# Performance work log

Measured on AMD Instinct MI355X. Metric: run time of the kernel, lower is better.

The kernel has to match this reference:

```python
import jax, jax.numpy as jnp
import numpy as np

N, E = 16384, 262144
IN, H, OUT = 128, 256, 256
L, HEADS = 4, 8
OC = H // HEADS  # 32, also MHA head_dim
B, NB = 64, 256  # graphs, nodes per graph (N = B*NB, equal-size graphs)


def _ln(x, g, b, eps=1e-5):
    m = x.mean(-1, keepdims=True)
    v = ((x - m) ** 2).mean(-1, keepdims=True)
    return (x - m) / jnp.sqrt(v + eps) * g + b


def setup_inputs() -> dict:
    key = jax.random.key(0)
    ks = iter(jax.random.split(key, 40))
    r = lambda *s: jax.random.normal(next(ks), s, jnp.float32) * 0.05
    return dict(
        x=jax.random.normal(next(ks), (N, IN), jnp.float32),
        edge_index=jax.random.randint(next(ks), (2, E), 0, N),
        wi=r(IN, H), bi=r(H),
        wg=r(L, H, H), asrc=r(L, HEADS, OC), adst=r(L, HEADS, OC), bg=r(L, H),
        g1=jnp.ones((L, H)), b1=jnp.zeros((L, H)),
        inw=r(L, 3 * H, H), inb=r(L, 3 * H), ow=r(L, H, H), ob=r(L, H),
        g2=jnp.ones((L, H)), b2=jnp.zeros((L, H)),
        mw1=r(L, H, 2 * H), mb1=r(L, 2 * H), mw2=r(L, 2 * H, H), mb2=r(L, H),
        g3=jnp.ones((L, H)), b3=jnp.zeros((L, H)),
        gf=jnp.ones(H), bf=jnp.zeros(H),
        wo=r(H, OUT), bo=r(OUT),
    )


def reference(x, edge_index, wi, bi, wg, asrc, adst, bg, g1, b1, inw, inb,
              ow, ob, g2, b2, mw1, mb1, mw2, mb2, g3, b3, gf, bf, wo, bo):
    src, dst = edge_index[0], edge_index[1]
    x = jax.nn.relu(x @ wi + bi)  # [N, H]
    for i in range(L):
        # ---- GATConv (local MPNN), eval mode (no dropout) ----
        xw = (x @ wg[i]).reshape(N, HEADS, OC)
        a = (xw * asrc[i]).sum(-1)[src] + (xw * adst[i]).sum(-1)[dst]  # [E, HEADS]
        a = jax.nn.leaky_relu(a, 0.2)
        amax = jax.ops.segment_max(a, dst, num_segments=N)
        ae = jnp.exp(a - amax[dst])
        asum = jax.ops.segment_sum(ae, dst, num_segments=N)
        attn = ae / asum[dst]  # edge softmax per destination node
        h = jax.ops.segment_sum(attn[:, :, None] * xw[src], dst, num_segments=N)
        h = h.reshape(N, H) + bg[i]
        h = _ln(h + x, g1[i], b1[i])  # GPSConv local branch + residual + norm1
        # ---- global MultiheadAttention over dense batch (equal-size graphs) ----
        xd = x.reshape(B, NB, H)
        qkv = xd @ inw[i].T + inb[i]
        q, k, v = jnp.split(qkv, 3, axis=-1)
        q = q.reshape(B, NB, HEADS, OC).transpose(0, 2, 1, 3)
        k = k.reshape(B, NB, HEADS, OC).transpose(0, 2, 1, 3)
        v = v.reshape(B, NB, HEADS, OC).transpose(0, 2, 1, 3)
        p = jax.nn.softmax(jnp.einsum('bhqd,bhkd->bhqk', q, k) / jnp.sqrt(jnp.float32(OC)), axis=-1)
        o = jnp.einsum('bhqk,bhkd->bhqd', p, v).transpose(0, 2, 1, 3).reshape(B, NB, H)
        o = (o @ ow[i].T + ob[i]).reshape(N, H)
        h2 = _ln(o + x, g2[i], b2[i])  # global branch + residual + norm2
        out = h + h2
        out = out + (jax.nn.relu(out @ mw1[i] + mb1[i]) @ mw2[i] + mb2[i])  # MLP residual
        x = _ln(out, g3[i], b3[i])  # norm3
    x = _ln(x, gf, bf)
    return x @ wo + bo
```

## Files before the change

kernel.cpp:

```cpp
#include <hip/hip_runtime.h>
#include <hip/hip_bf16.h>

#define NNODES 16384
#define NEDGES 262144
#define IND    128
#define HD     256
#define OUTDIM 256
#define LAYERS 4
#define NHEADS 8
#define OCD    32
#define NGRAPH 64
#define NBATCH 256
#define XQSTR  1024

typedef __hip_bfloat16 bf16;
typedef __attribute__((ext_vector_type(8))) short bf16x8;
typedef __attribute__((ext_vector_type(4))) short s16x4;
typedef __attribute__((ext_vector_type(4))) float f32x4;

__device__ __forceinline__ short bfbits(float v) {
    bf16 h = __float2bfloat16(v);
    return *(short*)&h;
}
__device__ __forceinline__ float b2f(short s) {
    return __uint_as_float(((unsigned)(unsigned short)s) << 16);
}

__device__ __forceinline__ size_t bidx(int row, int col, int KC) {
    return ((size_t)((row >> 6) * KC + (col >> 3)) << 9) + ((row & 63) << 3) + (col & 7);
}

__device__ __forceinline__ void gload_lds16(const short* g, short* l) {
    __builtin_amdgcn_global_load_lds(
        (const __attribute__((address_space(1))) void*)g,
        (__attribute__((address_space(3))) void*)l, 16, 0, 0);
}

#define PREP_TOTAL (32768 + NNODES*IND + IND*HD + LAYERS*1024*HD + LAYERS*1024 \
                    + LAYERS*HD*HD + LAYERS*HD*2*HD + LAYERS*2*HD*HD + HD*OUTDIM)
__global__ void prep_kernel(const float* __restrict__ x0, const float* __restrict__ wi,
                            const float* __restrict__ inw, const float* __restrict__ wg,
                            const float* __restrict__ inb, const float* __restrict__ ow,
                            const float* __restrict__ mw1, const float* __restrict__ mw2,
                            const float* __restrict__ wo,
                            short* __restrict__ x016, short* __restrict__ wi_t,
                            short* __restrict__ wcomb, float* __restrict__ cbias,
                            short* __restrict__ ow_c, short* __restrict__ mw1_t,
                            short* __restrict__ mw2_t, short* __restrict__ wo_t,
                            int* __restrict__ cnt, int* __restrict__ fill)
{
    int i = blockIdx.x * blockDim.x + threadIdx.x;
    if (i < 32768) {
        if (i < NNODES) cnt[i] = 0; else fill[i - NNODES] = 0;
        return;
    }
    i -= 32768;
    if (i < NNODES * IND) {
        int row = i / IND, col = i % IND;
        x016[bidx(row, col, 16)] = bfbits(x0[i]);
        return;
    }
    i -= NNODES * IND;
    if (i < IND * HD) {
        int k = i / HD, n = i % HD;
        wi_t[bidx(n, k, 16)] = bfbits(wi[i]);
        return;
    }
    i -= IND * HD;
    if (i < LAYERS * 1024 * HD) {
        int l = i >> 18, r = (i >> 8) & 1023, k = i & 255;
        float v = (r < 768) ? inw[(size_t)l * 768 * 256 + r * 256 + k]
                            : wg[(size_t)l * 256 * 256 + k * 256 + (r - 768)];
        wcomb[((size_t)l << 18) + bidx(r, k, 32)] = bfbits(v);
        return;
    }
    i -= LAYERS * 1024 * HD;
    if (i < LAYERS * 1024) {
        int l = i >> 10, c = i & 1023;
        cbias[i] = (c < 768) ? inb[l * 768 + c] : 0.f;
        return;
    }
    i -= LAYERS * 1024;
    if (i < LAYERS * HD * HD) {
        int l = i >> 16, rem = i & 65535, r = rem >> 8, k = rem & 255;
        ow_c[((size_t)l << 16) + bidx(r, k, 32)] = bfbits(ow[i]);
        return;
    }
    i -= LAYERS * HD * HD;
    if (i < LAYERS * HD * 2 * HD) {
        int l = i / (HD * 2 * HD), rem = i % (HD * 2 * HD);
        int k = rem / (2 * HD), n = rem % (2 * HD);
        mw1_t[(size_t)l * HD * 2 * HD + bidx(n, k, 32)] = bfbits(mw1[i]);
        return;
    }
    i -= LAYERS * HD * 2 * HD;
    if (i < LAYERS * 2 * HD * HD) {
        int l = i / (2 * HD * HD), rem = i % (2 * HD * HD);
        int k = rem / HD, n = rem % HD;
        mw2_t[(size_t)l * 2 * HD * HD + bidx(n, k, 64)] = bfbits(mw2[i]);
        return;
    }
    i -= LAYERS * 2 * HD * HD;
    if (i < HD * OUTDIM) {
        int k = i / OUTDIM, n = i % OUTDIM;
        wo_t[bidx(n, k, 32)] = bfbits(wo[i]);
    }
}

__global__ void hist_kernel(const int* __restrict__ dst, int* __restrict__ cnt)
{
    int e = blockIdx.x * blockDim.x + threadIdx.x;
    if (e < NEDGES) atomicAdd(&cnt[dst[e]], 1);
}

__global__ void scan_kernel(const int* __restrict__ cnt, int* __restrict__ row_ptr)
{
    __shared__ int part[256];
    int t = threadIdx.x;
    const int PER = NNODES / 256;
    int base = t * PER;
    int s = 0;
    for (int i = 0; i < PER; i++) s += cnt[base + i];
    part[t] = s;
    __syncthreads();
    for (int off = 1; off < 256; off <<= 1) {
        int v = (t >= off) ? part[t - off] : 0;
        __syncthreads();
        part[t] += v;
        __syncthreads();
    }
    int run = (t == 0) ? 0 : part[t - 1];
    for (int i = 0; i < PER; i++) { row_ptr[base + i] = run; run += cnt[base + i]; }
    if (t == 255) row_ptr[NNODES] = run;
}

__global__ void scatter_kernel(const int* __restrict__ src, const int* __restrict__ dst,
                               const int* __restrict__ row_ptr, int* __restrict__ fill,
                               int* __restrict__ srcs)
{
    int e = blockIdx.x * blockDim.x + threadIdx.x;
    if (e >= NEDGES) return;
    int d = dst[e];
    int pos = row_ptr[d] + atomicAdd(&fill[d], 1);
    srcs[pos] = src[e];
}

__global__ void gat_scores_kernel(const short* __restrict__ xw16,
                                  const float* __restrict__ asrc, const float* __restrict__ adst,
                                  float* __restrict__ ssrc, float* __restrict__ sdst)
{
    int i = blockIdx.x * blockDim.x + threadIdx.x;
    if (i >= NNODES * NHEADS) return;
    int n = i >> 3, h = i & 7;
    const bf16x8* xr = (const bf16x8*)(xw16 + (size_t)n * XQSTR + h * OCD);
    float s1 = 0.f, s2 = 0.f;
#pragma unroll
    for (int g = 0; g < 4; g++) {
        bf16x8 v8 = xr[g];
#pragma unroll
        for (int j = 0; j < 8; j++) {
            float v = b2f(v8[j]);
            int d = g * 8 + j;
            s1 += v * asrc[h * OCD + d];
            s2 += v * adst[h * OCD + d];
        }
    }
    ssrc[i] = s1;
    sdst[i] = s2;
}

__global__ __launch_bounds__(256)
void gat_agg_ln_kernel(const int* __restrict__ row_ptr, const int* __restrict__ srcs,
                       const float* __restrict__ ssrc, const float* __restrict__ sdst,
                       const short* __restrict__ xw16, const float* __restrict__ xcur,
                       const float* __restrict__ colbias, const float* __restrict__ gamma,
                       const float* __restrict__ beta, float* __restrict__ out)
{
    int wave = threadIdx.x >> 6, lane = threadIdx.x & 63;
    int n = blockIdx.x * 4 + wave;
    int c0 = lane << 2;
    int h = c0 >> 5;
    int start = row_ptr[n];
    int deg = row_ptr[n + 1] - start;
    float sd = sdst[n * NHEADS + h];

    float ax = 0.f, ay = 0.f, az = 0.f, aw = 0.f, l = 0.f;
    int j = 0;
    for (; j + 4 <= deg; j += 4) {
        int e0 = srcs[start + j + 0], e1 = srcs[start + j + 1];
        int e2 = srcs[start + j + 2], e3 = srcs[start + j + 3];
        s16x4 r0 = *(const s16x4*)&xw16[(size_t)e0 * XQSTR + c0];
        s16x4 r1 = *(const s16x4*)&xw16[(size_t)e1 * XQSTR + c0];
        s16x4 r2 = *(const s16x4*)&xw16[(size_t)e2 * XQSTR + c0];
        s16x4 r3 = *(const s16x4*)&xw16[(size_t)e3 * XQSTR + c0];
        float a0 = ssrc[e0 * NHEADS + h] + sd; a0 = a0 > 0.f ? a0 : 0.2f * a0;
        float a1 = ssrc[e1 * NHEADS + h] + sd; a1 = a1 > 0.f ? a1 : 0.2f * a1;
        float a2 = ssrc[e2 * NHEADS + h] + sd; a2 = a2 > 0.f ? a2 : 0.2f * a2;
        float a3 = ssrc[e3 * NHEADS + h] + sd; a3 = a3 > 0.f ? a3 : 0.2f * a3;
        float p0 = __expf(a0), p1 = __expf(a1), p2 = __expf(a2), p3 = __expf(a3);
        l += (p0 + p1) + (p2 + p3);
        ax += p0 * b2f(r0[0]) + p1 * b2f(r1[0]) + p2 * b2f(r2[0]) + p3 * b2f(r3[0]);
        ay += p0 * b2f(r0[1]) + p1 * b2f(r1[1]) + p2 * b2f(r2[1]) + p3 * b2f(r3[1]);
        az += p0 * b2f(r0[2]) + p1 * b2f(r1[2]) + p2 * b2f(r2[2]) + p3 * b2f(r3[2]);
        aw += p0 * b2f(r0[3]) + p1 * b2f(r1[3]) + p2 * b2f(r2[3]) + p3 * b2f(r3[3]);
    }
    for (; j < deg; j++) {
        int e0 = srcs[start + j];
        s16x4 r0 = *(const s16x4*)&xw16[(size_t)e0 * XQSTR + c0];
        float a0 = ssrc[e0 * NHEADS + h] + sd; a0 = a0 > 0.f ? a0 : 0.2f * a0;
        float p0 = __expf(a0);
        l += p0;
        ax += p0 * b2f(r0[0]); ay += p0 * b2f(r0[1]);
        az += p0 * b2f(r0[2]); aw += p0 * b2f(r0[3]);
    }
    float invl = deg ? 1.f / l : 0.f;
    size_t base = (size_t)n * HD + c0;
    float4 x4 = *(const float4*)&xcur[base];
    float4 cb = *(const float4*)&colbias[c0];
    float4 v;
    v.x = ax * invl + x4.x + cb.x;
    v.y = ay * invl + x4.y + cb.y;
    v.z = az * invl + x4.z + cb.z;
    v.w = aw * invl + x4.w + cb.w;
    float s = v.x + v.y + v.z + v.w;
    float q = v.x * v.x + v.y * v.y + v.z * v.z + v.w * v.w;
#pragma unroll
    for (int off = 1; off < 64; off <<= 1) {
        s += __shfl_xor(s, off);
        q += __shfl_xor(q, off);
    }
    float mean = s * (1.f / HD);
    float var  = fmaxf(q * (1.f / HD) - mean * mean, 0.f);
    float inv  = rsqrtf(var + 1e-5f);
    float4 g  = *(const float4*)&gamma[c0];
    float4 bt = *(const float4*)&beta[c0];
    float4 y;
    y.x = (v.x - mean) * inv * g.x + bt.x;
    y.y = (v.y - mean) * inv * g.y + bt.y;
    y.z = (v.z - mean) * inv * g.z + bt.z;
    y.w = (v.w - mean) * inv * g.w + bt.w;
    *(float4*)&out[base] = y;
}

#define GBM 128
#define GBK 32

template<int TN>
__global__ __launch_bounds__(256)
void gemm_mfma_kernel(const short* __restrict__ A16, const short* __restrict__ B16,
                      const float* __restrict__ bias, const float* __restrict__ resid,
                      float* __restrict__ Cf, short* __restrict__ C16,
                      int M, int Nc, int K, int relu, int c16rm)
{
    constexpr int NTF = TN / 32;
    __shared__ short As[GBM * GBK];
    __shared__ short Bs[TN * GBK];
    int tid = threadIdx.x;
    int wid = tid >> 6, lane = tid & 63;
    int quad = lane >> 4, l16 = lane & 15;
    int wm = wid >> 1, wn = wid & 1;
    int rowBase = blockIdx.y * GBM;
    int colBase = blockIdx.x * TN;
    int KC = K >> 3;

    f32x4 acc[4][NTF];
#pragma unroll
    for (int mt = 0; mt < 4; mt++)
#pragma unroll
        for (int nt = 0; nt < NTF; nt++) acc[mt][nt] = (f32x4)(0.f);

    const short* Ag0 = A16 + (((size_t)(blockIdx.y * 2 + 0) * KC + wid) << 9) + lane * 8;
    const short* Ag1 = A16 + (((size_t)(blockIdx.y * 2 + 1) * KC + wid) << 9) + lane * 8;
    const short* Bg0 = B16 + (((size_t)((colBase >> 6) + 0) * KC + wid) << 9) + lane * 8;
    const short* Bg1 = (TN == 128) ?
        B16 + (((size_t)((colBase >> 6) + 1) * KC + wid) << 9) + lane * 8 : nullptr;
    short* AsD0 = As + (wid * 128 + 0) * 8;
    short* AsD1 = As + (wid * 128 + 64) * 8;
    short* BsD0 = Bs + (wid * TN) * 8;
    short* BsD1 = Bs + (wid * TN + 64) * 8;

    for (int t = 0; t < (K >> 5); t++) {
        gload_lds16(Ag0 + t * 2048, AsD0);
        gload_lds16(Ag1 + t * 2048, AsD1);
        gload_lds16(Bg0 + t * 2048, BsD0);
        if (TN == 128) gload_lds16(Bg1 + t * 2048, BsD1);
        __syncthreads();
        bf16x8 aF[4], bF[NTF];
#pragma unroll
        for (int mt = 0; mt < 4; mt++)
            aF[mt] = *(bf16x8*)&As[(quad * 128 + wm * 64 + mt * 16 + l16) * 8];
#pragma unroll
        for (int nt = 0; nt < NTF; nt++)
            bF[nt] = *(bf16x8*)&Bs[(quad * TN + wn * (TN / 2) + nt * 16 + l16) * 8];
#pragma unroll
        for (int mt = 0; mt < 4; mt++)
#pragma unroll
            for (int nt = 0; nt < NTF; nt++)
                acc[mt][nt] = __builtin_amdgcn_mfma_f32_16x16x32_bf16(
                    bF[nt], aF[mt], acc[mt][nt], 0, 0, 0);
        __syncthreads();
    }

#pragma unroll
    for (int mt = 0; mt < 4; mt++) {
        int row = rowBase + wm * 64 + mt * 16 + l16;
#pragma unroll
        for (int nt = 0; nt < NTF; nt++) {
            int col0 = colBase + wn * (TN / 2) + nt * 16 + quad * 4;
            f32x4 v = acc[mt][nt];
            if (bias) {
                float4 b4 = *(const float4*)&bias[col0];
                v[0] += b4.x; v[1] += b4.y; v[2] += b4.z; v[3] += b4.w;
            }
            if (resid) {
                float4 r4 = *(const float4*)&resid[(size_t)row * Nc + col0];
                v[0] += r4.x; v[1] += r4.y; v[2] += r4.z; v[3] += r4.w;
            }
            if (relu) {
                v[0] = fmaxf(v[0], 0.f); v[1] = fmaxf(v[1], 0.f);
                v[2] = fmaxf(v[2], 0.f); v[3] = fmaxf(v[3], 0.f);
            }
            if (Cf) {
                float4 o; o.x = v[0]; o.y = v[1]; o.z = v[2]; o.w = v[3];
                *(float4*)&Cf[(size_t)row * Nc + col0] = o;
            }
            if (C16) {
                s16x4 o;
                o[0] = bfbits(v[0]); o[1] = bfbits(v[1]);
                o[2] = bfbits(v[2]); o[3] = bfbits(v[3]);
                if (c16rm) *(s16x4*)&C16[(size_t)row * Nc + col0] = o;
                else       *(s16x4*)&C16[bidx(row, col0, Nc >> 3)] = o;
            }
        }
    }
}

__global__ __launch_bounds__(256)
void gemm_ln_kernel(const short* __restrict__ A16, const short* __restrict__ B16,
                    const float* __restrict__ bias, const float* __restrict__ resid,
                    const float* __restrict__ gamma, const float* __restrict__ beta,
                    const float* __restrict__ postadd,
                    float* __restrict__ outf, short* __restrict__ out16, int K)
{
    __shared__ short As[64 * GBK];
    __shared__ short Bs[256 * GBK];
    int tid = threadIdx.x;
    int wid = tid >> 6, lane = tid & 63;
    int quad = lane >> 4, l16 = lane & 15;
    int rowBase = blockIdx.y * 64;
    int KC = K >> 3;

    f32x4 acc[16];
#pragma unroll
    for (int nt = 0; nt < 16; nt++) acc[nt] = (f32x4)(0.f);

    const short* Ag  = A16 + (((size_t)blockIdx.y * KC + wid) << 9) + lane * 8;
    const short* Bg0 = B16 + (((size_t)0 * KC + wid) << 9) + lane * 8;
    const short* Bg1 = B16 + (((size_t)1 * KC + wid) << 9) + lane * 8;
    const short* Bg2 = B16 + (((size_t)2 * KC + wid) << 9) + lane * 8;
    const short* Bg3 = B16 + (((size_t)3 * KC + wid) << 9) + lane * 8;
    short* AsD  = As + (wid * 64) * 8;
    short* BsD0 = Bs + (wid * 256 + 0) * 8;
    short* BsD1 = Bs + (wid * 256 + 64) * 8;
    short* BsD2 = Bs + (wid * 256 + 128) * 8;
    short* BsD3 = Bs + (wid * 256 + 192) * 8;

    for (int t = 0; t < (K >> 5); t++) {
        gload_lds16(Ag + t * 2048, AsD);
        gload_lds16(Bg0 + t * 2048, BsD0);
        gload_lds16(Bg1 + t * 2048, BsD1);
        gload_lds16(Bg2 + t * 2048, BsD2);
        gload_lds16(Bg3 + t * 2048, BsD3);
        __syncthreads();
        bf16x8 aF = *(bf16x8*)&As[(quad * 64 + wid * 16 + l16) * 8];
#pragma unroll
        for (int nt = 0; nt < 16; nt++) {
            bf16x8 bF = *(bf16x8*)&Bs[(quad * 256 + nt * 16 + l16) * 8];
            acc[nt] = __builtin_amdgcn_mfma_f32_16x16x32_bf16(bF, aF, acc[nt], 0, 0, 0);
        }
        __syncthreads();
    }

    int row = rowBase + wid * 16 + l16;
    float s = 0.f, q = 0.f;
#pragma unroll
    for (int nt = 0; nt < 16; nt++) {
        int col0 = nt * 16 + quad * 4;
        f32x4 v = acc[nt];
        float4 b4 = *(const float4*)&bias[col0];
        float4 r4 = *(const float4*)&resid[(size_t)row * HD + col0];
        v[0] += b4.x + r4.x; v[1] += b4.y + r4.y;
        v[2] += b4.z + r4.z; v[3] += b4.w + r4.w;
        acc[nt] = v;
        s += (v[0] + v[1]) + (v[2] + v[3]);
        q += (v[0] * v[0] + v[1] * v[1]) + (v[2] * v[2] + v[3] * v[3]);
    }
    s += __shfl_xor(s, 16); s += __shfl_xor(s, 32);
    q += __shfl_xor(q, 16); q += __shfl_xor(q, 32);
    float mean = s * (1.f / HD);
    float var  = fmaxf(q * (1.f / HD) - mean * mean, 0.f);
    float inv  = rsqrtf(var + 1e-5f);
#pragma unroll
    for (int nt = 0; nt < 16; nt++) {
        int col0 = nt * 16 + quad * 4;
        f32x4 v = acc[nt];
        float4 g4 = *(const float4*)&gamma[col0];
        float4 bt = *(const float4*)&beta[col0];
        float4 y;
        y.x = (v[0] - mean) * inv * g4.x + bt.x;
        y.y = (v[1] - mean) * inv * g4.y + bt.y;
        y.z = (v[2] - mean) * inv * g4.z + bt.z;
        y.w = (v[3] - mean) * inv * g4.w + bt.w;
        if (postadd) {
            float4 p4 = *(const float4*)&postadd[(size_t)row * HD + col0];
            y.x += p4.x; y.y += p4.y; y.z += p4.z; y.w += p4.w;
        }
        *(float4*)&outf[(size_t)row * HD + col0] = y;
        s16x4 o;
        o[0] = bfbits(y.x); o[1] = bfbits(y.y); o[2] = bfbits(y.z); o[3] = bfbits(y.w);
        *(s16x4*)&out16[bidx(row, col0, 32)] = o;
    }
}

__global__ __launch_bounds__(256)
void ln4_kernel(const float* __restrict__ in, const float* __restrict__ res,
                const float* __restrict__ gamma, const float* __restrict__ beta,
                const float* __restrict__ postadd,
                float* __restrict__ outf, short* __restrict__ out16)
{
    int wave = threadIdx.x >> 6, lane = threadIdx.x & 63;
    int row = blockIdx.x * 4 + wave;
    size_t base = (size_t)row * HD + lane * 4;
    float4 v = *(const float4*)&in[base];
    if (res) {
        float4 r = *(const float4*)&res[base];
        v.x += r.x; v.y += r.y; v.z += r.z; v.w += r.w;
    }
    float s = v.x + v.y + v.z + v.w;
    float q = v.x * v.x + v.y * v.y + v.z * v.z + v.w * v.w;
#pragma unroll
    for (int off = 1; off < 64; off <<= 1) {
        s += __shfl_xor(s, off);
        q += __shfl_xor(q, off);
    }
    float mean = s * (1.f / HD);
    float var  = fmaxf(q * (1.f / HD) - mean * mean, 0.f);
    float inv  = rsqrtf(var + 1e-5f);
    float4 g  = *(const float4*)&gamma[lane * 4];
    float4 bt = *(const float4*)&beta[lane * 4];
    float4 y;
    y.x = (v.x - mean) * inv * g.x + bt.x;
    y.y = (v.y - mean) * inv * g.y + bt.y;
    y.z = (v.z - mean) * inv * g.z + bt.z;
    y.w = (v.w - mean) * inv * g.w + bt.w;
    if (postadd) {
        float4 p = *(const float4*)&postadd[base];
        y.x += p.x; y.y += p.y; y.z += p.z; y.w += p.w;
    }
    if (outf) *(float4*)&outf[base] = y;
    if (out16) {
        s16x4 o;
        o[0] = bfbits(y.x); o[1] = bfbits(y.y); o[2] = bfbits(y.z); o[3] = bfbits(y.w);
        *(s16x4*)&out16[bidx(row, lane * 4, 32)] = o;
    }
}

#define PSTR 72
__global__ __launch_bounds__(256)
void mha_mfma_kernel(const short* __restrict__ qkv16, short* __restrict__ o16)
{
    __shared__ short smem[4 * 64 * PSTR + 32 * PSTR];
    short* VT = smem + 4 * 64 * PSTR;

    int b = blockIdx.x, h = blockIdx.y;
    int tid = threadIdx.x;
    int wid = tid >> 6, lane = tid & 63;
    int quad = lane >> 4, l16 = lane & 15;
    int base = b * NBATCH;
    int qrow0 = wid * 64;
    short* Pme = smem + wid * 64 * PSTR;

    const float scale2 = 0.17677669529663687f * 1.4426950408889634f;

    bf16x8 qA[4];
#pragma unroll
    for (int mt = 0; mt < 4; mt++)
        qA[mt] = *(const bf16x8*)&qkv16[(size_t)(base + qrow0 + mt * 16 + l16) * XQSTR + h * 32 + quad * 8];

    f32x4 accO[4][2];
#pragma unroll
    for (int mt = 0; mt < 4; mt++)
#pragma unroll
        for (int dt = 0; dt < 2; dt++) accO[mt][dt] = (f32x4)(0.f);
    float lsum[4][4];
#pragma unroll
    for (int mt = 0; mt < 4; mt++)
#pragma unroll
        for (int r = 0; r < 4; r++) lsum[mt][r] = 0.f;

    for (int c = 0; c < 4; c++) {
        __syncthreads();
        {
            int key = tid >> 2, dq = (tid & 3) * 8;
            bf16x8 v = *(const bf16x8*)&qkv16[(size_t)(base + c * 64 + key) * XQSTR + 512 + h * 32 + dq];
#pragma unroll
            for (int j = 0; j < 8; j++) VT[(dq + j) * PSTR + key] = v[j];
        }
        __syncthreads();
        bf16x8 kB[4];
#pragma unroll
        for (int kt = 0; kt < 4; kt++)
            kB[kt] = *(const bf16x8*)&qkv16[(size_t)(base + c * 64 + kt * 16 + l16) * XQSTR + 256 + h * 32 + quad * 8];
#pragma unroll
        for (int mt = 0; mt < 4; mt++) {
#pragma unroll
            for (int kt = 0; kt < 4; kt++) {
                f32x4 s = __builtin_amdgcn_mfma_f32_16x16x32_bf16(qA[mt], kB[kt], (f32x4)(0.f), 0, 0, 0);
#pragma unroll
                for (int r = 0; r < 4; r++) {
                    float p = exp2f(s[r] * scale2);
                    lsum[mt][r] += p;
                    Pme[(mt * 16 + quad * 4 + r) * PSTR + kt * 16 + l16] = bfbits(p);
                }
            }
        }
        __syncthreads();
#pragma unroll
        for (int mt = 0; mt < 4; mt++) {
#pragma unroll
            for (int ks = 0; ks < 2; ks++) {
                bf16x8 pA = *(bf16x8*)&Pme[(mt * 16 + l16) * PSTR + ks * 32 + quad * 8];
#pragma unroll
                for (int dt = 0; dt < 2; dt++) {
                    bf16x8 vB = *(bf16x8*)&VT[(dt * 16 + l16) * PSTR + ks * 32 + quad * 8];
                    accO[mt][dt] = __builtin_amdgcn_mfma_f32_16x16x32_bf16(pA, vB, accO[mt][dt], 0, 0, 0);
                }
            }
        }
    }
#pragma unroll
    for (int mt = 0; mt < 4; mt++)
#pragma unroll
        for (int r = 0; r < 4; r++) {
            float v = lsum[mt][r];
            v += __shfl_xor(v, 1);
            v += __shfl_xor(v, 2);
            v += __shfl_xor(v, 4);
            v += __shfl_xor(v, 8);
            lsum[mt][r] = v;
        }
#pragma unroll
    for (int mt = 0; mt < 4; mt++)
#pragma unroll
        for (int dt = 0; dt < 2; dt++)
#pragma unroll
            for (int r = 0; r < 4; r++) {
                int row = base + qrow0 + mt * 16 + quad * 4 + r;
                int col = h * 32 + dt * 16 + l16;
                o16[bidx(row, col, 32)] = bfbits(accO[mt][dt][r] / lsum[mt][r]);
            }
}

extern "C" void kernel_launch(void* const* d_in, const int* in_sizes, int n_in,
                              void* d_out, int out_size, void* d_ws, size_t ws_size,
                              hipStream_t stream)
{
    const float* x0   = (const float*)d_in[0];
    const int*   ei   = (const int*)d_in[1];
    const float* wi   = (const float*)d_in[2];
    const float* bi   = (const float*)d_in[3];
    const float* wg   = (const float*)d_in[4];
    const float* asrc = (const float*)d_in[5];
    const float* adst = (const float*)d_in[6];
    const float* bg   = (const float*)d_in[7];
    const float* g1   = (const float*)d_in[8];
    const float* b1   = (const float*)d_in[9];
    const float* inw  = (const float*)d_in[10];
    const float* inb  = (const float*)d_in[11];
    const float* ow   = (const float*)d_in[12];
    const float* ob   = (const float*)d_in[13];
    const float* g2   = (const float*)d_in[14];
    const float* b2   = (const float*)d_in[15];
    const float* mw1  = (const float*)d_in[16];
    const float* mb1  = (const float*)d_in[17];
    const float* mw2  = (const float*)d_in[18];
    const float* mb2  = (const float*)d_in[19];
    const float* g3   = (const float*)d_in[20];
    const float* b3   = (const float*)d_in[21];
    const float* gf   = (const float*)d_in[22];
    const float* bf_  = (const float*)d_in[23];
    const float* wo   = (const float*)d_in[24];
    const float* bo   = (const float*)d_in[25];

    const int* srcI = ei;
    const int* dstI = ei + NEDGES;

    const size_t NH = (size_t)NNODES * HD;
    float* ws   = (float*)d_ws;
    float* xcur = ws;
    float* xw   = xcur + NH;
    float* hbuf = xw + NH;
    float* obuf = hbuf + NH;
    float* qkvb = obuf + NH;
    int*   srcs    = (int*)(qkvb + 3 * NH);
    int*   row_ptr = srcs + NEDGES;
    int*   cnt     = row_ptr + NNODES + 1;
    int*   fill    = cnt + NNODES;
    float* ssrc    = (float*)(fill + NNODES);
    float* sdst    = ssrc + (size_t)NNODES * NHEADS;
    short* xq16   = (short*)qkvb;
    short* x016   = (short*)(sdst + (size_t)NNODES * NHEADS);
    short* xcur16 = x016 + (size_t)NNODES * IND;
    short* b16a   = xcur16 + NH;
    short* hid16  = b16a + NH;
    short* wi_t  = hid16 + 2 * NH;
    short* wcomb = wi_t + (size_t)HD * IND;
    short* ow_c  = wcomb + (size_t)LAYERS * 1024 * HD;
    short* mw1_t = ow_c + (size_t)LAYERS * HD * HD;
    short* mw2_t = mw1_t + (size_t)LAYERS * HD * 2 * HD;
    short* wo_t  = mw2_t + (size_t)LAYERS * 2 * HD * HD;
    float* cbias = (float*)(wo_t + (size_t)HD * OUTDIM);

    const int T = 256;
    const int nNH = NNODES * NHEADS;

    prep_kernel<<<(PREP_TOTAL + T - 1) / T, T, 0, stream>>>(
        x0, wi, inw, wg, inb, ow, mw1, mw2, wo,
        x016, wi_t, wcomb, cbias, ow_c, mw1_t, mw2_t, wo_t, cnt, fill);

    hist_kernel<<<(NEDGES + T - 1) / T, T, 0, stream>>>(dstI, cnt);
    scan_kernel<<<1, 256, 0, stream>>>(cnt, row_ptr);
    scatter_kernel<<<(NEDGES + T - 1) / T, T, 0, stream>>>(srcI, dstI, row_ptr, fill, srcs);

    gemm_mfma_kernel<64><<<dim3(HD / 64, NNODES / GBM), 256, 0, stream>>>(
        x016, wi_t, bi, nullptr, xcur, xcur16, NNODES, HD, IND, 1, 0);

    for (int i = 0; i < LAYERS; i++) {
        const float* asrc_i = asrc + (size_t)i * NHEADS * OCD;
        const float* adst_i = adst + (size_t)i * NHEADS * OCD;
        const float* bg_i   = bg + (size_t)i * HD;
        const float* g1_i   = g1 + (size_t)i * HD;
        const float* b1_i   = b1 + (size_t)i * HD;
        const float* ob_i   = ob + (size_t)i * HD;
        const float* g2_i   = g2 + (size_t)i * HD;
        const float* b2_i   = b2 + (size_t)i * HD;
        const float* mb1_i  = mb1 + (size_t)i * 2 * HD;
        const float* mb2_i  = mb2 + (size_t)i * HD;
        const float* g3_i   = g3 + (size_t)i * HD;
        const float* b3_i   = b3 + (size_t)i * HD;
        const short* wcomb_i = wcomb + (size_t)i * 1024 * HD;
        const float* cbias_i = cbias + (size_t)i * 1024;
        const short* ow_ci  = ow_c + (size_t)i * HD * HD;
        const short* mw1_ti = mw1_t + (size_t)i * HD * 2 * HD;
        const short* mw2_ti = mw2_t + (size_t)i * 2 * HD * HD;

        gemm_mfma_kernel<128><<<dim3(1024 / 128, NNODES / GBM), 256, 0, stream>>>(
            xcur16, wcomb_i, cbias_i, nullptr, nullptr, xq16, NNODES, 1024, HD, 0, 1);

        gat_scores_kernel<<<(nNH + T - 1) / T, T, 0, stream>>>(xq16 + 768, asrc_i, adst_i, ssrc, sdst);
        gat_agg_ln_kernel<<<NNODES / 4, 256, 0, stream>>>(
            row_ptr, srcs, ssrc, sdst, xq16 + 768, xcur, bg_i, g1_i, b1_i, hbuf);

        mha_mfma_kernel<<<dim3(NGRAPH, NHEADS), 256, 0, stream>>>(xq16, b16a);
        gemm_ln_kernel<<<dim3(1, NNODES / 64), 256, 0, stream>>>(
            b16a, ow_ci, ob_i, xcur, g2_i, b2_i, hbuf, obuf, b16a, HD);

        gemm_mfma_kernel<128><<<dim3(2 * HD / 128, NNODES / GBM), 256, 0, stream>>>(
            b16a, mw1_ti, mb1_i, nullptr, nullptr, hid16, NNODES, 2 * HD, HD, 1, 0);
        gemm_ln_kernel<<<dim3(1, NNODES / 64), 256, 0, stream>>>(
            hid16, mw2_ti, mb2_i, obuf, g3_i, b3_i, nullptr, xcur, xcur16, 2 * HD);
    }

    ln4_kernel<<<NNODES / 4, 256, 0, stream>>>(xcur, nullptr, gf, bf_, nullptr, nullptr, b16a);
    gemm_mfma_kernel<64><<<dim3(OUTDIM / 64, NNODES / GBM), 256, 0, stream>>>(
        b16a, wo_t, bo, nullptr, (float*)d_out, nullptr, NNODES, OUTDIM, HD, 0, 0);
}
```

Measured before the change: 749.4 us.

## Double-buffer LDS tiles in GEMM kernels and unroll GAT aggregation by eight

Both MFMA GEMM kernels (the generic tiled one and the fused GEMM+LayerNorm one) now use two LDS buffers. The next K-tile's global-to-LDS load is issued right after the barrier, before the current tile is computed, and the trailing barrier is dropped, so each iteration has one sync. This is meant to overlap memory latency with MFMA work, at the cost of twice the shared memory per block, which may lower occupancy. Separately, the GAT neighbour aggregation loop is unrolled from 4 to 8 edges, with all index, feature and score loads issued before the math to expose more memory-level parallelism, at the cost of more registers.

```diff
diff --git a/kernel.cpp b/kernel.cpp
--- a/kernel.cpp
+++ b/kernel.cpp
@@ -186,23 +186,27 @@
 
     float ax = 0.f, ay = 0.f, az = 0.f, aw = 0.f, l = 0.f;
     int j = 0;
-    for (; j + 4 <= deg; j += 4) {
-        int e0 = srcs[start + j + 0], e1 = srcs[start + j + 1];
-        int e2 = srcs[start + j + 2], e3 = srcs[start + j + 3];
-        s16x4 r0 = *(const s16x4*)&xw16[(size_t)e0 * XQSTR + c0];
-        s16x4 r1 = *(const s16x4*)&xw16[(size_t)e1 * XQSTR + c0];
-        s16x4 r2 = *(const s16x4*)&xw16[(size_t)e2 * XQSTR + c0];
-        s16x4 r3 = *(const s16x4*)&xw16[(size_t)e3 * XQSTR + c0];
-        float a0 = ssrc[e0 * NHEADS + h] + sd; a0 = a0 > 0.f ? a0 : 0.2f * a0;
-        float a1 = ssrc[e1 * NHEADS + h] + sd; a1 = a1 > 0.f ? a1 : 0.2f * a1;
-        float a2 = ssrc[e2 * NHEADS + h] + sd; a2 = a2 > 0.f ? a2 : 0.2f * a2;
-        float a3 = ssrc[e3 * NHEADS + h] + sd; a3 = a3 > 0.f ? a3 : 0.2f * a3;
-        float p0 = __expf(a0), p1 = __expf(a1), p2 = __expf(a2), p3 = __expf(a3);
-        l += (p0 + p1) + (p2 + p3);
-        ax += p0 * b2f(r0[0]) + p1 * b2f(r1[0]) + p2 * b2f(r2[0]) + p3 * b2f(r3[0]);
-        ay += p0 * b2f(r0[1]) + p1 * b2f(r1[1]) + p2 * b2f(r2[1]) + p3 * b2f(r3[1]);
-        az += p0 * b2f(r0[2]) + p1 * b2f(r1[2]) + p2 * b2f(r2[2]) + p3 * b2f(r3[2]);
-        aw += p0 * b2f(r0[3]) + p1 * b2f(r1[3]) + p2 * b2f(r2[3]) + p3 * b2f(r3[3]);
+    for (; j + 8 <= deg; j += 8) {
+        int e[8];
+        s16x4 r[8];
+        float sc[8];
+#pragma unroll
+        for (int u = 0; u < 8; u++) e[u] = srcs[start + j + u];
+#pragma unroll
+        for (int u = 0; u < 8; u++) r[u] = *(const s16x4*)&xw16[(size_t)e[u] * XQSTR + c0];
+#pragma unroll
+        for (int u = 0; u < 8; u++) sc[u] = ssrc[e[u] * NHEADS + h];
+#pragma unroll
+        for (int u = 0; u < 8; u++) {
+            float a = sc[u] + sd;
+            a = a > 0.f ? a : 0.2f * a;
+            float p = __expf(a);
+            l += p;
+            ax += p * b2f(r[u][0]);
+            ay += p * b2f(r[u][1]);
+            az += p * b2f(r[u][2]);
+            aw += p * b2f(r[u][3]);
+        }
     }
     for (; j < deg; j++) {
         int e0 = srcs[start + j];
@@ -253,8 +257,10 @@
                       int M, int Nc, int K, int relu, int c16rm)
 {
     constexpr int NTF = TN / 32;
-    __shared__ short As[GBM * GBK];
-    __shared__ short Bs[TN * GBK];
+    constexpr int ASZ = GBM * GBK;
+    constexpr int BSZ = TN * GBK;
+    __shared__ short As[2 * ASZ];
+    __shared__ short Bs[2 * BSZ];
     int tid = threadIdx.x;
     int wid = tid >> 6, lane = tid & 63;
     int quad = lane >> 4, l16 = lane & 15;
@@ -279,26 +285,37 @@
     short* BsD0 = Bs + (wid * TN) * 8;
     short* BsD1 = Bs + (wid * TN + 64) * 8;
 
-    for (int t = 0; t < (K >> 5); t++) {
-        gload_lds16(Ag0 + t * 2048, AsD0);
-        gload_lds16(Ag1 + t * 2048, AsD1);
-        gload_lds16(Bg0 + t * 2048, BsD0);
-        if (TN == 128) gload_lds16(Bg1 + t * 2048, BsD1);
+    int TT = K >> 5;
+    gload_lds16(Ag0, AsD0);
+    gload_lds16(Ag1, AsD1);
+    gload_lds16(Bg0, BsD0);
+    if (TN == 128) gload_lds16(Bg1, BsD1);
+
+    for (int t = 0; t < TT; t++) {
         __syncthreads();
+        int cur = t & 1;
+        if (t + 1 < TT) {
+            int nb = (t + 1) & 1;
+            gload_lds16(Ag0 + (t + 1) * 2048, AsD0 + nb * ASZ);
+            gload_lds16(Ag1 + (t + 1) * 2048, AsD1 + nb * ASZ);
+            gload_lds16(Bg0 + (t + 1) * 2048, BsD0 + nb * BSZ);
+            if (TN == 128) gload_lds16(Bg1 + (t + 1) * 2048, BsD1 + nb * BSZ);
+        }
+        const short* Ab = As + cur * ASZ;
+        const short* Bb = Bs + cur * BSZ;
         bf16x8 aF[4], bF[NTF];
 #pragma unroll
         for (int mt = 0; mt < 4; mt++)
-            aF[mt] = *(bf16x8*)&As[(quad * 128 + wm * 64 + mt * 16 + l16) * 8];
+            aF[mt] = *(bf16x8*)&Ab[(quad * 128 + wm * 64 + mt * 16 + l16) * 8];
 #pragma unroll
         for (int nt = 0; nt < NTF; nt++)
-            bF[nt] = *(bf16x8*)&Bs[(quad * TN + wn * (TN / 2) + nt * 16 + l16) * 8];
+            bF[nt] = *(bf16x8*)&Bb[(quad * TN + wn * (TN / 2) + nt * 16 + l16) * 8];
 #pragma unroll
         for (int mt = 0; mt < 4; mt++)
 #pragma unroll
             for (int nt = 0; nt < NTF; nt++)
                 acc[mt][nt] = __builtin_amdgcn_mfma_f32_16x16x32_bf16(
                     bF[nt], aF[mt], acc[mt][nt], 0, 0, 0);
-        __syncthreads();
     }
 
 #pragma unroll
@@ -342,8 +359,10 @@
                     const float* __restrict__ postadd,
                     float* __restrict__ outf, short* __restrict__ out16, int K)
 {
-    __shared__ short As[64 * GBK];
-    __shared__ short Bs[256 * GBK];
+    constexpr int ASZ = 64 * GBK;
+    constexpr int BSZ = 256 * GBK;
+    __shared__ short As[2 * ASZ];
+    __shared__ short Bs[2 * BSZ];
     int tid = threadIdx.x;
     int wid = tid >> 6, lane = tid & 63;
     int quad = lane >> 4, l16 = lane & 15;
@@ -365,20 +384,32 @@
     short* BsD2 = Bs + (wid * 256 + 128) * 8;
     short* BsD3 = Bs + (wid * 256 + 192) * 8;
 
-    for (int t = 0; t < (K >> 5); t++) {
-        gload_lds16(Ag + t * 2048, AsD);
-        gload_lds16(Bg0 + t * 2048, BsD0);
-        gload_lds16(Bg1 + t * 2048, BsD1);
-        gload_lds16(Bg2 + t * 2048, BsD2);
-        gload_lds16(Bg3 + t * 2048, BsD3);
+    int TT = K >> 5;
+    gload_lds16(Ag, AsD);
+    gload_lds16(Bg0, BsD0);
+    gload_lds16(Bg1, BsD1);
+    gload_lds16(Bg2, BsD2);
+    gload_lds16(Bg3, BsD3);
+
+    for (int t = 0; t < TT; t++) {
         __syncthreads();
-        bf16x8 aF = *(bf16x8*)&As[(quad * 64 + wid * 16 + l16) * 8];
+        int cur = t & 1;
+        if (t + 1 < TT) {
+            int nb = (t + 1) & 1;
+            gload_lds16(Ag + (t + 1) * 2048, AsD + nb * ASZ);
+            gload_lds16(Bg0 + (t + 1) * 2048, BsD0 + nb * BSZ);
+            gload_lds16(Bg1 + (t + 1) * 2048, BsD1 + nb * BSZ);
+            gload_lds16(Bg2 + (t + 1) * 2048, BsD2 + nb * BSZ);
+            gload_lds16(Bg3 + (t + 1) * 2048, BsD3 + nb * BSZ);
+        }
+        const short* Ab = As + cur * ASZ;
+        const short* Bb = Bs + cur * BSZ;
+        bf16x8 aF = *(bf16x8*)&Ab[(quad * 64 + wid * 16 + l16) * 8];
 #pragma unroll
         for (int nt = 0; nt < 16; nt++) {
-            bf16x8 bF = *(bf16x8*)&Bs[(quad * 256 + nt * 16 + l16) * 8];
+            bf16x8 bF = *(bf16x8*)&Bb[(quad * 256 + nt * 16 + l16) * 8];
             acc[nt] = __builtin_amdgcn_mfma_f32_16x16x32_bf16(bF, aF, acc[nt], 0, 0, 0);
         }
-        __syncthreads();
     }
 
     int row = rowBase + wid * 16 + l16;
```

Result: faster. 732.9 us (-2.2%).
